# Kernel optimization log

Measured on AMD Instinct MI355X. Metric: run time of the kernel, lower is better.

The kernel has to match this reference:

```python
import jax, jax.numpy as jnp
import numpy as np

TEXT_DIM = 1024
FEAT_DIM = 1024
NUM_HEADS = 16
HEAD_DIM = FEAT_DIM // NUM_HEADS
EPS = 1e-6


def rms_norm(x, w):
    # LlamaRMSNorm: compute in fp32, scale by learned weight
    xf = x.astype(jnp.float32)
    var = jnp.mean(xf * xf, axis=-1, keepdims=True)
    return (xf * jax.lax.rsqrt(var + EPS)).astype(x.dtype) * w


def setup_inputs() -> dict:
    key = jax.random.key(0)
    ks = jax.random.split(key, 8)
    def xavier(k, shape, gain=1.0):
        fan_in, fan_out = shape[1], shape[0]
        lim = gain * np.sqrt(6.0 / (fan_in + fan_out))
        return jax.random.uniform(k, shape, jnp.float32, -lim, lim)
    return {
        "text": jax.random.normal(ks[0], (8, 512, TEXT_DIM), jnp.float32),
        "features": jax.random.normal(ks[1], (8, 1024, FEAT_DIM), jnp.float32),
        "W_q": xavier(ks[2], (FEAT_DIM, TEXT_DIM)),
        "b_q": jnp.zeros((FEAT_DIM,), jnp.float32),
        "W_k": xavier(ks[3], (FEAT_DIM, FEAT_DIM)),
        "b_k": jnp.zeros((FEAT_DIM,), jnp.float32),
        "W_o": xavier(ks[4], (FEAT_DIM, FEAT_DIM), gain=0.1),
        "b_o": jnp.zeros((FEAT_DIM,), jnp.float32),
        "g_feat": jnp.ones((FEAT_DIM,), jnp.float32),
        "g_q": jnp.ones((FEAT_DIM,), jnp.float32),
        "g_k": jnp.ones((FEAT_DIM,), jnp.float32),
    }


def reference(text, features, W_q, b_q, W_k, b_k, W_o, b_o, g_feat, g_q, g_k):
    B, T, _ = text.shape
    _, N, _ = features.shape
    feats = rms_norm(features, g_feat)                      # [B,N,Df]
    Q = rms_norm(text @ W_q.T + b_q, g_q)                   # [B,T,Df]
    K = rms_norm(feats @ W_k.T + b_k, g_k)                  # [B,N,Df]
    Qh = Q.reshape(B, T, NUM_HEADS, HEAD_DIM)
    Kh = K.reshape(B, N, NUM_HEADS, HEAD_DIM)
    Vh = feats.reshape(B, N, NUM_HEADS, HEAD_DIM)
    scores = jnp.einsum("bthd,bnhd->bhtn", Qh, Kh) / np.sqrt(HEAD_DIM).astype(np.float32)
    attn = jax.nn.softmax(scores, axis=-1)                  # [B,H,T,N]
    out = jnp.einsum("bhtn,bnhd->bthd", attn, Vh).reshape(B, T, FEAT_DIM)
    return out @ W_o.T + b_o
```

## Files before the change

### kernel.cpp

```cpp
#include <hip/hip_runtime.h>
#include <hip/hip_bf16.h>


typedef unsigned short u16;
typedef __bf16 bf16x8 __attribute__((ext_vector_type(8)));
typedef float f32x4 __attribute__((ext_vector_type(4)));

__device__ inline f32x4 mfma16(bf16x8 a, bf16x8 b, f32x4 c) {
    return __builtin_amdgcn_mfma_f32_16x16x32_bf16(a, b, c, 0, 0, 0);
}

__device__ inline u16 f2bf(float f) {
    union { float f; unsigned u; } v; v.f = f;
    unsigned r = v.u + 0x7fffu + ((v.u >> 16) & 1u);
    return (u16)(r >> 16);
}

__device__ inline float bf2f(u16 x) {
    union { unsigned u; float f; } v; v.u = ((unsigned)x) << 16; return v.f;
}

__device__ inline unsigned pk_bf16(float a, float b) {
    union { float f; unsigned u; } x, y; x.f = a; y.f = b;
    return __builtin_amdgcn_perm(y.u + 0x8000u, x.u + 0x8000u, 0x07060302u);
}

__device__ inline void load_lds16(const void* g, void* l) {
    __builtin_amdgcn_global_load_lds(
        (const __attribute__((address_space(1))) void*)g,
        (__attribute__((address_space(3))) void*)l, 16, 0, 0);
}

__global__ __launch_bounds__(256) void cast4_kernel(const float* __restrict__ text,
                                                    const float* __restrict__ Wq,
                                                    const float* __restrict__ Wk,
                                                    const float* __restrict__ Wo,
                                                    u16* __restrict__ otext, u16* __restrict__ oWq,
                                                    u16* __restrict__ oWk, u16* __restrict__ oWo) {
    int i = blockIdx.x * 256 + threadIdx.x;
    const float* src; u16* dst; int off;
    if (i < 1048576)      { src = text; dst = otext; off = i; }
    else if (i < 1310720) { src = Wq;   dst = oWq;   off = i - 1048576; }
    else if (i < 1572864) { src = Wk;   dst = oWk;   off = i - 1310720; }
    else                  { src = Wo;   dst = oWo;   off = i - 1572864; }
    float4 v = ((const float4*)src)[off];
    uint2 p; p.x = pk_bf16(v.x, v.y); p.y = pk_bf16(v.z, v.w);
    ((uint2*)dst)[off] = p;
}

__global__ __launch_bounds__(256) void rmsnorm_kernel(const float* __restrict__ in,
                                                      const float* __restrict__ g,
                                                      u16* __restrict__ out, float scale) {
    int row = blockIdx.x, tid = threadIdx.x;
    float4 v = ((const float4*)(in + (size_t)row * 1024))[tid];
    float ss = v.x * v.x + v.y * v.y + v.z * v.z + v.w * v.w;
    #pragma unroll
    for (int m = 1; m < 64; m <<= 1) ss += __shfl_xor(ss, m, 64);
    __shared__ float ws[4];
    if ((tid & 63) == 0) ws[tid >> 6] = ss;
    __syncthreads();
    float rs = rsqrtf((ws[0] + ws[1] + ws[2] + ws[3]) * (1.0f / 1024.0f) + 1e-6f) * scale;
    float4 gv = ((const float4*)g)[tid];
    uint2 p;
    p.x = pk_bf16(v.x * rs * gv.x, v.y * rs * gv.y);
    p.y = pk_bf16(v.z * rs * gv.z, v.w * rs * gv.w);
    ((uint2*)(out + (size_t)row * 1024))[tid] = p;
}

__global__ __launch_bounds__(256) void rmsnorm_qk_kernel(u16* __restrict__ QK,
                                                         const float* __restrict__ g_q,
                                                         const float* __restrict__ g_k,
                                                         float qscale) {
    int row = blockIdx.x, tid = threadIdx.x;
    const float* g = (row < 4096) ? g_q : g_k;
    float outsc = (row < 4096) ? qscale : 1.0f;
    uint2* rp = (uint2*)(QK + (size_t)row * 1024) + tid;
    union { u16 s[4]; uint2 v; } in; in.v = *rp;
    float x0 = bf2f(in.s[0]), x1 = bf2f(in.s[1]), x2 = bf2f(in.s[2]), x3 = bf2f(in.s[3]);
    float ss = x0 * x0 + x1 * x1 + x2 * x2 + x3 * x3;
    #pragma unroll
    for (int m = 1; m < 64; m <<= 1) ss += __shfl_xor(ss, m, 64);
    __shared__ float ws[4];
    if ((tid & 63) == 0) ws[tid >> 6] = ss;
    __syncthreads();
    float rs = rsqrtf((ws[0] + ws[1] + ws[2] + ws[3]) * (1.0f / 1024.0f) + 1e-6f) * outsc;
    float4 gv = ((const float4*)g)[tid];
    uint2 p;
    p.x = pk_bf16(x0 * rs * gv.x, x1 * rs * gv.y);
    p.y = pk_bf16(x2 * rs * gv.z, x3 * rs * gv.w);
    *rp = p;
}

__global__ __launch_bounds__(256) void transpose_kernel(const u16* __restrict__ in,
                                                        u16* __restrict__ out) {
    __shared__ __align__(16) u16 tile[64][72];
    int tid = threadIdx.x, b = blockIdx.z;
    int n0 = blockIdx.x * 64, d0 = blockIdx.y * 64;
    int r = tid >> 2, cs = (tid & 3) * 16;
    const u16* src = in + ((size_t)(b * 1024 + n0 + r)) * 1024 + d0 + cs;
    union { u16 s[8]; uint4 v; } a0, a1;
    a0.v = *(const uint4*)src;
    a1.v = *(const uint4*)(src + 8);
    #pragma unroll
    for (int i = 0; i < 8; ++i) { tile[r][cs + i] = a0.s[i]; tile[r][cs + 8 + i] = a1.s[i]; }
    __syncthreads();
    union { u16 s[8]; uint4 v; } b0, b1;
    #pragma unroll
    for (int i = 0; i < 8; ++i) { b0.s[i] = tile[cs + i][r]; b1.s[i] = tile[cs + 8 + i][r]; }
    u16* dst = out + ((size_t)(b * 1024 + d0 + r)) * 1024 + n0 + cs;
    *(uint4*)dst = b0.v;
    *(uint4*)(dst + 8) = b1.v;
}

template <bool BF16OUT>
__device__ __forceinline__ void gemm64_tile(const u16* __restrict__ A, const u16* __restrict__ B,
                                            const float* __restrict__ bias, void* __restrict__ Cout,
                                            int m_blk, int n_blk, int K, int N,
                                            u16* As, u16* Bs) {
    int tid = threadIdx.x, wave = tid >> 6, lane = tid & 63;
    int quad = lane >> 4, l15 = lane & 15;
    int wm = wave & 1, wn = wave >> 1;

    f32x4 acc[4][2] = {};

    for (int k0 = 0; k0 < K; k0 += 32) {
        #pragma unroll
        for (int j = 0; j < 2; ++j) {
            int idx = j * 256 + tid;
            int row = idx >> 2, kc = (idx & 3) * 8;
            load_lds16(A + (size_t)(m_blk + row) * K + k0 + kc, As + (j * 256 + wave * 64) * 8);
        }
        {
            int row = tid >> 2, kc = (tid & 3) * 8;
            load_lds16(B + (size_t)(n_blk + row) * K + k0 + kc, Bs + (wave * 64) * 8);
        }
        __syncthreads();
        bf16x8 af[4], bfr[2];
        #pragma unroll
        for (int t = 0; t < 4; ++t)
            af[t] = *(const bf16x8*)&As[(wm * 64 + t * 16 + l15) * 32 + quad * 8];
        #pragma unroll
        for (int t = 0; t < 2; ++t)
            bfr[t] = *(const bf16x8*)&Bs[(wn * 32 + t * 16 + l15) * 32 + quad * 8];
        #pragma unroll
        for (int mt = 0; mt < 4; ++mt)
            #pragma unroll
            for (int nt = 0; nt < 2; ++nt)
                acc[mt][nt] = mfma16(af[mt], bfr[nt], acc[mt][nt]);
        __syncthreads();
    }
    #pragma unroll
    for (int nt = 0; nt < 2; ++nt) {
        int col = n_blk + wn * 32 + nt * 16 + l15;
        float bv = bias[col];
        #pragma unroll
        for (int mt = 0; mt < 4; ++mt) {
            int row0 = m_blk + wm * 64 + mt * 16 + quad * 4;
            #pragma unroll
            for (int r = 0; r < 4; ++r) {
                float val = acc[mt][nt][r] + bv;
                if (BF16OUT) ((u16*)Cout)[(size_t)(row0 + r) * N + col] = f2bf(val);
                else       ((float*)Cout)[(size_t)(row0 + r) * N + col] = val;
            }
        }
    }
}

__global__ __launch_bounds__(256) void gemm_qk_kernel(const u16* __restrict__ text_bf,
                                                      const u16* __restrict__ Wq,
                                                      const u16* __restrict__ feats_bf,
                                                      const u16* __restrict__ Wk,
                                                      const float* __restrict__ b_q,
                                                      const float* __restrict__ b_k,
                                                      u16* __restrict__ QK) {
    __shared__ __align__(16) u16 As[128 * 32];
    __shared__ __align__(16) u16 Bs[64 * 32];
    int id = blockIdx.x;
    if (id < 512) {
        gemm64_tile<true>(text_bf, Wq, b_q, QK, (id & 31) * 128, (id >> 5) * 64, 1024, 1024, As, Bs);
    } else {
        id -= 512;
        gemm64_tile<true>(feats_bf, Wk, b_k, QK + 4096 * 1024,
                          (id & 63) * 128, (id >> 6) * 64, 1024, 1024, As, Bs);
    }
}

__global__ __launch_bounds__(256) void gemm_o_kernel(const u16* __restrict__ A,
                                                     const u16* __restrict__ B,
                                                     const float* __restrict__ bias,
                                                     float* __restrict__ C) {
    __shared__ __align__(16) u16 As[128 * 32];
    __shared__ __align__(16) u16 Bs[64 * 32];
    int id = blockIdx.x;
    gemm64_tile<false>(A, B, bias, C, (id & 31) * 128, (id >> 5) * 64, 1024, 1024, As, Bs);
}

__global__ __launch_bounds__(256) void attn_kernel(const u16* __restrict__ Q,
                                                   const u16* __restrict__ K,
                                                   const u16* __restrict__ Vt,
                                                   u16* __restrict__ Out) {
    int bh = blockIdx.x, qt = blockIdx.y;
    int b = bh >> 4, h = bh & 15;
    int tid = threadIdx.x, wave = tid >> 6, lane = tid & 63;
    int quad = lane >> 4, l15 = lane & 15;

    __shared__ __align__(16) u16 Ks[64 * 64];
    __shared__ __align__(16) u16 Vs[64 * 64];
    __shared__ __align__(16) u16 Plds[4][16 * 72];
    u16* Pw = &Plds[wave][0];

    const size_t qoff = ((size_t)(b * 512 + qt * 64 + wave * 16 + l15)) * 1024 + h * 64 + quad * 8;
    bf16x8 qf0 = *(const bf16x8*)(Q + qoff);
    bf16x8 qf1 = *(const bf16x8*)(Q + qoff + 32);

    int srl = lane >> 3, scl = lane & 7;
    const u16* Kbase = K + ((size_t)(b * 1024)) * 1024 + h * 64;
    const u16* Vbase = Vt + ((size_t)(b * 1024 + h * 64)) * 1024;

    __bf16 onev = (__bf16)1.0f;
    bf16x8 ones = {onev, onev, onev, onev, onev, onev, onev, onev};

    f32x4 o[4] = {};
    f32x4 lac = {0.0f, 0.0f, 0.0f, 0.0f};

    for (int n0 = 0; n0 < 1024; n0 += 64) {
        #pragma unroll
        for (int j = 0; j < 2; ++j) {
            int row = wave * 16 + j * 8 + srl;
            load_lds16(Kbase + (size_t)(n0 + row) * 1024 + (scl ^ srl) * 8,
                       Ks + (wave * 16 + j * 8) * 64);
            load_lds16(Vbase + (size_t)row * 1024 + n0 + (scl ^ srl) * 8,
                       Vs + (wave * 16 + j * 8) * 64);
        }
        __syncthreads();

        f32x4 s[4];
        #pragma unroll
        for (int nt = 0; nt < 4; ++nt) {
            int R = nt * 16 + l15;
            int c1 = (quad ^ (l15 & 7)) * 8;
            bf16x8 kf0 = *(const bf16x8*)&Ks[R * 64 + c1];
            bf16x8 kf1 = *(const bf16x8*)&Ks[R * 64 + (c1 ^ 32)];
            f32x4 z = {-16.0f, -16.0f, -16.0f, -16.0f};
            s[nt] = mfma16(kf0, qf0, z);
            s[nt] = mfma16(kf1, qf1, s[nt]);
        }

        #pragma unroll
        for (int nt = 0; nt < 4; ++nt) {
            uint2 pk;
            pk.x = pk_bf16(exp2f(s[nt][0]), exp2f(s[nt][1]));
            pk.y = pk_bf16(exp2f(s[nt][2]), exp2f(s[nt][3]));
            *(uint2*)&Pw[l15 * 72 + nt * 16 + quad * 4] = pk;
        }

        bf16x8 pf[2];
        #pragma unroll
        for (int kc = 0; kc < 2; ++kc)
            pf[kc] = *(const bf16x8*)&Pw[l15 * 72 + kc * 32 + quad * 8];
        #pragma unroll
        for (int kc = 0; kc < 2; ++kc) {
            lac = mfma16(ones, pf[kc], lac);
            #pragma unroll
            for (int dt = 0; dt < 4; ++dt) {
                int d = dt * 16 + l15;
                int ch = ((kc * 4 + quad) ^ (l15 & 7)) * 8;
                bf16x8 vf = *(const bf16x8*)&Vs[d * 64 + ch];
                o[dt] = mfma16(vf, pf[kc], o[dt]);
            }
        }
        __syncthreads();
    }

    float il = 1.0f / lac[0];
    size_t obase = ((size_t)(b * 512 + qt * 64 + wave * 16 + l15)) * 1024 + h * 64 + quad * 4;
    #pragma unroll
    for (int dt = 0; dt < 4; ++dt) {
        uint2 pk;
        pk.x = pk_bf16(o[dt][0] * il, o[dt][1] * il);
        pk.y = pk_bf16(o[dt][2] * il, o[dt][3] * il);
        *(uint2*)(Out + obase + dt * 16) = pk;
    }
}

extern "C" void kernel_launch(void* const* d_in, const int* in_sizes, int n_in,
                              void* d_out, int out_size, void* d_ws, size_t ws_size,
                              hipStream_t stream) {
    const float* text     = (const float*)d_in[0];
    const float* features = (const float*)d_in[1];
    const float* W_q      = (const float*)d_in[2];
    const float* b_q      = (const float*)d_in[3];
    const float* W_k      = (const float*)d_in[4];
    const float* b_k      = (const float*)d_in[5];
    const float* W_o      = (const float*)d_in[6];
    const float* b_o      = (const float*)d_in[7];
    const float* g_feat   = (const float*)d_in[8];
    const float* g_q      = (const float*)d_in[9];
    const float* g_k      = (const float*)d_in[10];

    char* ws = (char*)d_ws;
    u16* text_bf  = (u16*)(ws + 0);
    u16* Wq_bf    = (u16*)(ws + 8388608);
    u16* Wk_bf    = (u16*)(ws + 10485760);
    u16* Wo_bf    = (u16*)(ws + 12582912);
    u16* feats_bf = (u16*)(ws + 14680064);
    u16* Vt       = (u16*)(ws + 31457280);
    u16* QKbuf    = (u16*)(ws + 48234496);
    u16* attn_bf  = (u16*)(ws + 73400320);

    const float QSCALE = 0.18033688011112042f;

    cast4_kernel<<<7168, 256, 0, stream>>>(text, W_q, W_k, W_o, text_bf, Wq_bf, Wk_bf, Wo_bf);

    rmsnorm_kernel<<<8192, 256, 0, stream>>>(features, g_feat, feats_bf, 1.0f);
    transpose_kernel<<<dim3(16, 16, 8), 256, 0, stream>>>(feats_bf, Vt);

    gemm_qk_kernel<<<1536, 256, 0, stream>>>(text_bf, Wq_bf, feats_bf, Wk_bf, b_q, b_k, QKbuf);
    rmsnorm_qk_kernel<<<12288, 256, 0, stream>>>(QKbuf, g_q, g_k, QSCALE);

    attn_kernel<<<dim3(128, 8), 256, 0, stream>>>(QKbuf, QKbuf + 4096 * 1024, Vt, attn_bf);

    gemm_o_kernel<<<512, 256, 0, stream>>>(attn_bf, Wo_bf, b_o, (float*)d_out);
}
```

Before: 237.7 us.

## Fuse feature norm with transpose, widen GEMM K-step, one wave per norm row

The feature RMS sum-of-squares moves into the cast kernel as extra blocks that write per-row sums to a workspace buffer. A new kernel then normalizes, writes bf16 features and the transposed V in one pass, replacing the separate rmsnorm and transpose kernels. The GEMM tile now loads a K-slab of 64 per iteration, which halves the barrier count at the cost of doubled LDS. The Q/K norm kernel handles one row per wave with 16 elements per lane and no block-level sync. The fused norm kernel reads the fp32 features a second time, so that input is read twice from memory.

```diff
diff --git a/kernel.cpp b/kernel.cpp
--- a/kernel.cpp
+++ b/kernel.cpp
@@ -31,122 +31,148 @@
         (__attribute__((address_space(3))) void*)l, 16, 0, 0);
 }
 
-__global__ __launch_bounds__(256) void cast4_kernel(const float* __restrict__ text,
-                                                    const float* __restrict__ Wq,
-                                                    const float* __restrict__ Wk,
-                                                    const float* __restrict__ Wo,
-                                                    u16* __restrict__ otext, u16* __restrict__ oWq,
-                                                    u16* __restrict__ oWk, u16* __restrict__ oWo) {
-    int i = blockIdx.x * 256 + threadIdx.x;
-    const float* src; u16* dst; int off;
-    if (i < 1048576)      { src = text; dst = otext; off = i; }
-    else if (i < 1310720) { src = Wq;   dst = oWq;   off = i - 1048576; }
-    else if (i < 1572864) { src = Wk;   dst = oWk;   off = i - 1310720; }
-    else                  { src = Wo;   dst = oWo;   off = i - 1572864; }
-    float4 v = ((const float4*)src)[off];
-    uint2 p; p.x = pk_bf16(v.x, v.y); p.y = pk_bf16(v.z, v.w);
-    ((uint2*)dst)[off] = p;
-}
-
-__global__ __launch_bounds__(256) void rmsnorm_kernel(const float* __restrict__ in,
-                                                      const float* __restrict__ g,
-                                                      u16* __restrict__ out, float scale) {
-    int row = blockIdx.x, tid = threadIdx.x;
-    float4 v = ((const float4*)(in + (size_t)row * 1024))[tid];
-    float ss = v.x * v.x + v.y * v.y + v.z * v.z + v.w * v.w;
-    #pragma unroll
-    for (int m = 1; m < 64; m <<= 1) ss += __shfl_xor(ss, m, 64);
-    __shared__ float ws[4];
-    if ((tid & 63) == 0) ws[tid >> 6] = ss;
+__global__ __launch_bounds__(256) void cast_rows_kernel(const float* __restrict__ text,
+                                                        const float* __restrict__ Wq,
+                                                        const float* __restrict__ Wk,
+                                                        const float* __restrict__ Wo,
+                                                        const float* __restrict__ features,
+                                                        u16* __restrict__ otext, u16* __restrict__ oWq,
+                                                        u16* __restrict__ oWk, u16* __restrict__ oWo,
+                                                        float* __restrict__ ssbuf) {
+    int blk = blockIdx.x, tid = threadIdx.x;
+    if (blk < 7168) {
+        int i = blk * 256 + tid;
+        const float* src; u16* dst; int off;
+        if (i < 1048576)      { src = text; dst = otext; off = i; }
+        else if (i < 1310720) { src = Wq;   dst = oWq;   off = i - 1048576; }
+        else if (i < 1572864) { src = Wk;   dst = oWk;   off = i - 1310720; }
+        else                  { src = Wo;   dst = oWo;   off = i - 1572864; }
+        float4 v = ((const float4*)src)[off];
+        uint2 p; p.x = pk_bf16(v.x, v.y); p.y = pk_bf16(v.z, v.w);
+        ((uint2*)dst)[off] = p;
+    } else {
+        int row = (blk - 7168) * 4 + (tid >> 6);
+        int lane = tid & 63;
+        const float4* rp = (const float4*)(features + (size_t)row * 1024) + lane * 4;
+        float ss = 0.0f;
+        #pragma unroll
+        for (int i = 0; i < 4; ++i) {
+            float4 v = rp[i];
+            ss += v.x * v.x + v.y * v.y + v.z * v.z + v.w * v.w;
+        }
+        #pragma unroll
+        for (int m = 1; m < 64; m <<= 1) ss += __shfl_xor(ss, m, 64);
+        if (lane == 0) ssbuf[row] = ss;
+    }
+}
+
+__global__ __launch_bounds__(256) void normT_kernel(const float* __restrict__ features,
+                                                    const float* __restrict__ ssbuf,
+                                                    const float* __restrict__ g,
+                                                    u16* __restrict__ feats_bf,
+                                                    u16* __restrict__ Vt) {
+    __shared__ __align__(16) u16 tile[64][72];
+    int tid = threadIdx.x, b = blockIdx.z;
+    int n0 = blockIdx.x * 64, d0 = blockIdx.y * 64;
+    int r = tid >> 2, cs = (tid & 3) * 16;
+    int grow = b * 1024 + n0 + r;
+
+    float rs = rsqrtf(ssbuf[grow] * (1.0f / 1024.0f) + 1e-6f);
+    const float4* src = (const float4*)(features + (size_t)grow * 1024 + d0 + cs);
+    const float4* gp  = (const float4*)(g + d0 + cs);
+    union { u16 s[16]; uint4 v[2]; } ob;
+    #pragma unroll
+    for (int i = 0; i < 4; ++i) {
+        float4 v = src[i], gv = gp[i];
+        unsigned lo = pk_bf16(v.x * rs * gv.x, v.y * rs * gv.y);
+        unsigned hi = pk_bf16(v.z * rs * gv.z, v.w * rs * gv.w);
+        ((unsigned*)ob.s)[i * 2]     = lo;
+        ((unsigned*)ob.s)[i * 2 + 1] = hi;
+    }
+    uint4* dst = (uint4*)(feats_bf + (size_t)grow * 1024 + d0 + cs);
+    dst[0] = ob.v[0]; dst[1] = ob.v[1];
+    #pragma unroll
+    for (int i = 0; i < 16; ++i) tile[r][cs + i] = ob.s[i];
     __syncthreads();
-    float rs = rsqrtf((ws[0] + ws[1] + ws[2] + ws[3]) * (1.0f / 1024.0f) + 1e-6f) * scale;
-    float4 gv = ((const float4*)g)[tid];
-    uint2 p;
-    p.x = pk_bf16(v.x * rs * gv.x, v.y * rs * gv.y);
-    p.y = pk_bf16(v.z * rs * gv.z, v.w * rs * gv.w);
-    ((uint2*)(out + (size_t)row * 1024))[tid] = p;
+    union { u16 s[8]; uint4 v; } t0, t1;
+    #pragma unroll
+    for (int i = 0; i < 8; ++i) { t0.s[i] = tile[cs + i][r]; t1.s[i] = tile[cs + 8 + i][r]; }
+    u16* tdst = Vt + ((size_t)(b * 1024 + d0 + r)) * 1024 + n0 + cs;
+    *(uint4*)tdst = t0.v;
+    *(uint4*)(tdst + 8) = t1.v;
 }
 
 __global__ __launch_bounds__(256) void rmsnorm_qk_kernel(u16* __restrict__ QK,
                                                          const float* __restrict__ g_q,
                                                          const float* __restrict__ g_k,
                                                          float qscale) {
-    int row = blockIdx.x, tid = threadIdx.x;
+    int tid = threadIdx.x;
+    int row = blockIdx.x * 4 + (tid >> 6);
+    int lane = tid & 63;
     const float* g = (row < 4096) ? g_q : g_k;
     float outsc = (row < 4096) ? qscale : 1.0f;
-    uint2* rp = (uint2*)(QK + (size_t)row * 1024) + tid;
-    union { u16 s[4]; uint2 v; } in; in.v = *rp;
-    float x0 = bf2f(in.s[0]), x1 = bf2f(in.s[1]), x2 = bf2f(in.s[2]), x3 = bf2f(in.s[3]);
-    float ss = x0 * x0 + x1 * x1 + x2 * x2 + x3 * x3;
+
+    u16* rp = QK + (size_t)row * 1024 + lane * 16;
+    union { u16 s[16]; uint4 v[2]; } in;
+    in.v[0] = *(const uint4*)rp;
+    in.v[1] = *(const uint4*)(rp + 8);
+    float x[16], ss = 0.0f;
+    #pragma unroll
+    for (int i = 0; i < 16; ++i) { x[i] = bf2f(in.s[i]); ss += x[i] * x[i]; }
     #pragma unroll
     for (int m = 1; m < 64; m <<= 1) ss += __shfl_xor(ss, m, 64);
-    __shared__ float ws[4];
-    if ((tid & 63) == 0) ws[tid >> 6] = ss;
-    __syncthreads();
-    float rs = rsqrtf((ws[0] + ws[1] + ws[2] + ws[3]) * (1.0f / 1024.0f) + 1e-6f) * outsc;
-    float4 gv = ((const float4*)g)[tid];
-    uint2 p;
-    p.x = pk_bf16(x0 * rs * gv.x, x1 * rs * gv.y);
-    p.y = pk_bf16(x2 * rs * gv.z, x3 * rs * gv.w);
-    *rp = p;
-}
-
-__global__ __launch_bounds__(256) void transpose_kernel(const u16* __restrict__ in,
-                                                        u16* __restrict__ out) {
-    __shared__ __align__(16) u16 tile[64][72];
-    int tid = threadIdx.x, b = blockIdx.z;
-    int n0 = blockIdx.x * 64, d0 = blockIdx.y * 64;
-    int r = tid >> 2, cs = (tid & 3) * 16;
-    const u16* src = in + ((size_t)(b * 1024 + n0 + r)) * 1024 + d0 + cs;
-    union { u16 s[8]; uint4 v; } a0, a1;
-    a0.v = *(const uint4*)src;
-    a1.v = *(const uint4*)(src + 8);
-    #pragma unroll
-    for (int i = 0; i < 8; ++i) { tile[r][cs + i] = a0.s[i]; tile[r][cs + 8 + i] = a1.s[i]; }
-    __syncthreads();
-    union { u16 s[8]; uint4 v; } b0, b1;
-    #pragma unroll
-    for (int i = 0; i < 8; ++i) { b0.s[i] = tile[cs + i][r]; b1.s[i] = tile[cs + 8 + i][r]; }
-    u16* dst = out + ((size_t)(b * 1024 + d0 + r)) * 1024 + n0 + cs;
-    *(uint4*)dst = b0.v;
-    *(uint4*)(dst + 8) = b1.v;
+    float rs = rsqrtf(ss * (1.0f / 1024.0f) + 1e-6f) * outsc;
+    const float4* gp = (const float4*)(g + lane * 16);
+    union { unsigned u[8]; uint4 v[2]; } ob;
+    #pragma unroll
+    for (int i = 0; i < 4; ++i) {
+        float4 gv = gp[i];
+        ob.u[i * 2]     = pk_bf16(x[i * 4 + 0] * rs * gv.x, x[i * 4 + 1] * rs * gv.y);
+        ob.u[i * 2 + 1] = pk_bf16(x[i * 4 + 2] * rs * gv.z, x[i * 4 + 3] * rs * gv.w);
+    }
+    *(uint4*)rp = ob.v[0];
+    *(uint4*)(rp + 8) = ob.v[1];
 }
 
 template <bool BF16OUT>
-__device__ __forceinline__ void gemm64_tile(const u16* __restrict__ A, const u16* __restrict__ B,
+__device__ __forceinline__ void gemm64_bk64(const u16* __restrict__ A, const u16* __restrict__ B,
                                             const float* __restrict__ bias, void* __restrict__ Cout,
                                             int m_blk, int n_blk, int K, int N,
                                             u16* As, u16* Bs) {
     int tid = threadIdx.x, wave = tid >> 6, lane = tid & 63;
     int quad = lane >> 4, l15 = lane & 15;
     int wm = wave & 1, wn = wave >> 1;
+    int arow = tid >> 2, ac = (tid & 3) * 8;
 
     f32x4 acc[4][2] = {};
 
-    for (int k0 = 0; k0 < K; k0 += 32) {
-        #pragma unroll
-        for (int j = 0; j < 2; ++j) {
-            int idx = j * 256 + tid;
-            int row = idx >> 2, kc = (idx & 3) * 8;
-            load_lds16(A + (size_t)(m_blk + row) * K + k0 + kc, As + (j * 256 + wave * 64) * 8);
-        }
-        {
-            int row = tid >> 2, kc = (tid & 3) * 8;
-            load_lds16(B + (size_t)(n_blk + row) * K + k0 + kc, Bs + (wave * 64) * 8);
-        }
+    for (int k0 = 0; k0 < K; k0 += 64) {
+        #pragma unroll
+        for (int kh = 0; kh < 2; ++kh)
+            #pragma unroll
+            for (int rh = 0; rh < 2; ++rh)
+                load_lds16(A + (size_t)(m_blk + rh * 64 + arow) * K + k0 + kh * 32 + ac,
+                           As + kh * 4096 + rh * 2048 + (wave * 64) * 8);
+        #pragma unroll
+        for (int kh = 0; kh < 2; ++kh)
+            load_lds16(B + (size_t)(n_blk + arow) * K + k0 + kh * 32 + ac,
+                       Bs + kh * 2048 + (wave * 64) * 8);
         __syncthreads();
-        bf16x8 af[4], bfr[2];
-        #pragma unroll
-        for (int t = 0; t < 4; ++t)
-            af[t] = *(const bf16x8*)&As[(wm * 64 + t * 16 + l15) * 32 + quad * 8];
-        #pragma unroll
-        for (int t = 0; t < 2; ++t)
-            bfr[t] = *(const bf16x8*)&Bs[(wn * 32 + t * 16 + l15) * 32 + quad * 8];
-        #pragma unroll
-        for (int mt = 0; mt < 4; ++mt)
-            #pragma unroll
-            for (int nt = 0; nt < 2; ++nt)
-                acc[mt][nt] = mfma16(af[mt], bfr[nt], acc[mt][nt]);
+        #pragma unroll
+        for (int kh = 0; kh < 2; ++kh) {
+            bf16x8 af[4], bfr[2];
+            #pragma unroll
+            for (int t = 0; t < 4; ++t)
+                af[t] = *(const bf16x8*)&As[kh * 4096 + (wm * 64 + t * 16 + l15) * 32 + quad * 8];
+            #pragma unroll
+            for (int t = 0; t < 2; ++t)
+                bfr[t] = *(const bf16x8*)&Bs[kh * 2048 + (wn * 32 + t * 16 + l15) * 32 + quad * 8];
+            #pragma unroll
+            for (int mt = 0; mt < 4; ++mt)
+                #pragma unroll
+                for (int nt = 0; nt < 2; ++nt)
+                    acc[mt][nt] = mfma16(af[mt], bfr[nt], acc[mt][nt]);
+        }
         __syncthreads();
     }
     #pragma unroll
@@ -173,14 +199,14 @@
                                                       const float* __restrict__ b_q,
                                                       const float* __restrict__ b_k,
                                                       u16* __restrict__ QK) {
-    __shared__ __align__(16) u16 As[128 * 32];
-    __shared__ __align__(16) u16 Bs[64 * 32];
+    __shared__ __align__(16) u16 As[2 * 128 * 32];
+    __shared__ __align__(16) u16 Bs[2 * 64 * 32];
     int id = blockIdx.x;
     if (id < 512) {
-        gemm64_tile<true>(text_bf, Wq, b_q, QK, (id & 31) * 128, (id >> 5) * 64, 1024, 1024, As, Bs);
+        gemm64_bk64<true>(text_bf, Wq, b_q, QK, (id & 31) * 128, (id >> 5) * 64, 1024, 1024, As, Bs);
     } else {
         id -= 512;
-        gemm64_tile<true>(feats_bf, Wk, b_k, QK + 4096 * 1024,
+        gemm64_bk64<true>(feats_bf, Wk, b_k, QK + 4096 * 1024,
                           (id & 63) * 128, (id >> 6) * 64, 1024, 1024, As, Bs);
     }
 }
@@ -189,10 +215,10 @@
                                                      const u16* __restrict__ B,
                                                      const float* __restrict__ bias,
                                                      float* __restrict__ C) {
-    __shared__ __align__(16) u16 As[128 * 32];
-    __shared__ __align__(16) u16 Bs[64 * 32];
+    __shared__ __align__(16) u16 As[2 * 128 * 32];
+    __shared__ __align__(16) u16 Bs[2 * 64 * 32];
     int id = blockIdx.x;
-    gemm64_tile<false>(A, B, bias, C, (id & 31) * 128, (id >> 5) * 64, 1024, 1024, As, Bs);
+    gemm64_bk64<false>(A, B, bias, C, (id & 31) * 128, (id >> 5) * 64, 1024, 1024, As, Bs);
 }
 
 __global__ __launch_bounds__(256) void attn_kernel(const u16* __restrict__ Q,
@@ -299,26 +325,23 @@
     const float* g_k      = (const float*)d_in[10];
 
     char* ws = (char*)d_ws;
-    u16* text_bf  = (u16*)(ws + 0);
-    u16* Wq_bf    = (u16*)(ws + 8388608);
-    u16* Wk_bf    = (u16*)(ws + 10485760);
-    u16* Wo_bf    = (u16*)(ws + 12582912);
-    u16* feats_bf = (u16*)(ws + 14680064);
-    u16* Vt       = (u16*)(ws + 31457280);
-    u16* QKbuf    = (u16*)(ws + 48234496);
-    u16* attn_bf  = (u16*)(ws + 73400320);
+    u16*   text_bf  = (u16*)(ws + 0);
+    u16*   Wq_bf    = (u16*)(ws + 8388608);
+    u16*   Wk_bf    = (u16*)(ws + 10485760);
+    u16*   Wo_bf    = (u16*)(ws + 12582912);
+    u16*   feats_bf = (u16*)(ws + 14680064);
+    u16*   Vt       = (u16*)(ws + 31457280);
+    u16*   QKbuf    = (u16*)(ws + 48234496);
+    u16*   attn_bf  = (u16*)(ws + 73400320);
+    float* ssbuf    = (float*)(ws + 81788928);
 
     const float QSCALE = 0.18033688011112042f;
 
-    cast4_kernel<<<7168, 256, 0, stream>>>(text, W_q, W_k, W_o, text_bf, Wq_bf, Wk_bf, Wo_bf);
-
-    rmsnorm_kernel<<<8192, 256, 0, stream>>>(features, g_feat, feats_bf, 1.0f);
-    transpose_kernel<<<dim3(16, 16, 8), 256, 0, stream>>>(feats_bf, Vt);
-
+    cast_rows_kernel<<<9216, 256, 0, stream>>>(text, W_q, W_k, W_o, features,
+                                               text_bf, Wq_bf, Wk_bf, Wo_bf, ssbuf);
+    normT_kernel<<<dim3(16, 16, 8), 256, 0, stream>>>(features, ssbuf, g_feat, feats_bf, Vt);
     gemm_qk_kernel<<<1536, 256, 0, stream>>>(text_bf, Wq_bf, feats_bf, Wk_bf, b_q, b_k, QKbuf);
-    rmsnorm_qk_kernel<<<12288, 256, 0, stream>>>(QKbuf, g_q, g_k, QSCALE);
-
+    rmsnorm_qk_kernel<<<3072, 256, 0, stream>>>(QKbuf, g_q, g_k, QSCALE);
     attn_kernel<<<dim3(128, 8), 256, 0, stream>>>(QKbuf, QKbuf + 4096 * 1024, Vt, attn_bf);
-
     gemm_o_kernel<<<512, 256, 0, stream>>>(attn_bf, Wo_bf, b_o, (float*)d_out);
 }
```

Measured after the change: 225.0 us. 1.06x faster.
